# Optimization experiments

Measured on AMD Instinct MI355X. Metric: run time of the kernel, lower is better.

The kernel has to match this reference:

```python
import jax, jax.numpy as jnp
import numpy as np

N_PAPER = 200000
N_MESH = 30000
N = N_PAPER + N_MESH
D_PAPER = 512
D_MESH = 128
E_TRAIN = 2000000
E_POS = 500000
E_NEG = 500000


def setup_inputs() -> dict:
    key = jax.random.key(0)
    ks = jax.random.split(key, 32)

    def w(k, shape, fan_in):
        return jax.random.normal(k, shape, jnp.float32) / np.float32(np.sqrt(fan_in))

    inp = {}
    inp['x_paper'] = jax.random.normal(ks[0], (N_PAPER, D_PAPER), jnp.float32)
    inp['x_mesh'] = jax.random.normal(ks[1], (N_MESH, D_MESH), jnp.float32)
    # input transforms (stored as [in, out]; y = x @ W + b)
    inp['tp_w'] = w(ks[2], (D_PAPER, 16), D_PAPER)
    inp['tp_b'] = jnp.zeros((16,), jnp.float32)
    inp['tm_w'] = w(ks[3], (D_MESH, 16), D_MESH)
    inp['tm_b'] = jnp.zeros((16,), jnp.float32)
    # RGCN layers: basis decomposition W_r = sum_b comp[r,b] * basis[b]
    inp['comp1'] = w(ks[4], (2, 4), 4)
    inp['basis1'] = w(ks[5], (4, 16, 32), 16)
    inp['root1'] = w(ks[6], (16, 32), 16)
    inp['bias1'] = jnp.zeros((32,), jnp.float32)
    inp['comp2'] = w(ks[7], (2, 4), 4)
    inp['basis2'] = w(ks[8], (4, 32, 32), 32)
    inp['root2'] = w(ks[9], (32, 32), 32)
    inp['bias2'] = jnp.zeros((32,), jnp.float32)
    inp['comp3'] = w(ks[10], (2, 4), 4)
    inp['basis3'] = w(ks[11], (4, 32, 16), 32)
    inp['root3'] = w(ks[12], (32, 16), 32)
    inp['bias3'] = jnp.zeros((16,), jnp.float32)
    # decode linears (16 -> 16)
    inp['dpp_w'] = w(ks[13], (16, 16), 16)
    inp['dpp_b'] = jnp.zeros((16,), jnp.float32)
    inp['dpm_w'] = w(ks[14], (16, 16), 16)
    inp['dpm_b'] = jnp.zeros((16,), jnp.float32)
    # graph structure
    inp['train_edge_index'] = jax.random.randint(ks[15], (2, E_TRAIN), 0, N, jnp.int64)
    inp['train_edge_type'] = jax.random.randint(ks[16], (E_TRAIN,), 0, 2, jnp.int64)
    inp['pos_edge_index'] = jax.random.randint(ks[17], (2, E_POS), 0, N, jnp.int64)
    inp['pos_edge_type'] = jnp.sort(jax.random.randint(ks[18], (E_POS,), 0, 2, jnp.int64))
    inp['neg_edge_index'] = jax.random.randint(ks[19], (2, E_NEG), 0, N, jnp.int64)
    inp['neg_edge_type'] = jnp.sort(jax.random.randint(ks[20], (E_NEG,), 0, 2, jnp.int64))
    return inp


def rgcn(x, src, dst, etype, comp, basis, root, bias):
    # W: [R, in, out] from basis decomposition
    W = jnp.einsum('rb,bio->rio', comp, basis)
    # relation-typed message per edge (R == 2: compute both, select)
    xs = x[src]                                   # [E, in]  gather
    m = jnp.where((etype == 0)[:, None], xs @ W[0], xs @ W[1])  # [E, out]
    n = x.shape[0]
    agg = jax.ops.segment_sum(m, dst, num_segments=n)           # scatter-add
    deg = jax.ops.segment_sum(jnp.ones((src.shape[0],), x.dtype), dst, num_segments=n)
    agg = agg / jnp.maximum(deg, 1.0)[:, None]                   # mean aggregation
    return agg + x @ root + bias


def reference(x_paper, x_mesh, tp_w, tp_b, tm_w, tm_b,
              comp1, basis1, root1, bias1,
              comp2, basis2, root2, bias2,
              comp3, basis3, root3, bias3,
              dpp_w, dpp_b, dpm_w, dpm_b,
              train_edge_index, train_edge_type,
              pos_edge_index, pos_edge_type,
              neg_edge_index, neg_edge_type):
    # encode
    x = jnp.concatenate([x_paper @ tp_w + tp_b, x_mesh @ tm_w + tm_b], axis=0)
    src, dst = train_edge_index[0], train_edge_index[1]
    x = jax.nn.relu(rgcn(x, src, dst, train_edge_type, comp1, basis1, root1, bias1))
    x = jax.nn.relu(rgcn(x, src, dst, train_edge_type, comp2, basis2, root2, bias2))
    z = rgcn(x, src, dst, train_edge_type, comp3, basis3, root3, bias3)

    # decode: edge types are sorted, so per-edge type-select equals the
    # original mask-then-concat ordering [type0 ..., type1 ...]
    def edge_scores(ei, et):
        zs, zd = z[ei[0]], z[ei[1]]
        p = jnp.where((et == 0)[:, None], zs @ dpp_w + dpp_b, zs @ dpm_w + dpm_b)
        return (p * zd).sum(-1)

    return jnp.concatenate([edge_scores(pos_edge_index, pos_edge_type),
                            edge_scores(neg_edge_index, neg_edge_type)], axis=0)
```

## Files before the change

kernel.cpp:

```cpp
#include <hip/hip_runtime.h>

#define NPAPER 200000
#define NMESH  30000
#define NNODES 230000
#define ETRAIN 2000000
#define EPOS   500000
#define ENEG   500000

typedef _Float16 f16;
typedef __attribute__((ext_vector_type(8))) _Float16 f16x8;
typedef __attribute__((ext_vector_type(4))) _Float16 f16x4;

__device__ __forceinline__ void fma4(float4& a, float s, const float4 w) {
    a.x = fmaf(s, w.x, a.x);
    a.y = fmaf(s, w.y, a.y);
    a.z = fmaf(s, w.z, a.z);
    a.w = fmaf(s, w.w, a.w);
}

template <int D>
__global__ __launch_bounds__(256) void encode_kernel(
    const float* __restrict__ x, const float* __restrict__ w,
    const float* __restrict__ bias, float* __restrict__ out, int nrows) {
    constexpr int KP = 16;
    __shared__ float wlds[D * 16];
    __shared__ float xlds[256 * 20];
    __shared__ float blds[16];

    for (int i = threadIdx.x; i < D * 4; i += 256)
        reinterpret_cast<float4*>(wlds)[i] =
            reinterpret_cast<const float4*>(w)[i];
    if (threadIdx.x < 16) blds[threadIdx.x] = bias[threadIdx.x];

    const int g = threadIdx.x & 3;
    const int rg = threadIdx.x >> 2;
    const int row0 = blockIdx.x * 256;

    float4 acc[4];
#pragma unroll
    for (int j = 0; j < 4; j++) acc[j] = make_float4(0.f, 0.f, 0.f, 0.f);

    for (int p = 0; p < D / KP; p++) {
        __syncthreads();
        for (int i = threadIdx.x; i < 1024; i += 256) {
            const int rr = i >> 2, q = i & 3;
            const int grow = min(row0 + rr, nrows - 1);
            *reinterpret_cast<float4*>(xlds + rr * 20 + q * 4) =
                *reinterpret_cast<const float4*>(x + (size_t)grow * D +
                                                 p * KP + q * 4);
        }
        __syncthreads();
#pragma unroll
        for (int q = 0; q < KP / 4; q++) {
            const int k = p * KP + q * 4;
            const float4 w0 =
                *reinterpret_cast<const float4*>(wlds + (k + 0) * 16 + 4 * g);
            const float4 w1 =
                *reinterpret_cast<const float4*>(wlds + (k + 1) * 16 + 4 * g);
            const float4 w2 =
                *reinterpret_cast<const float4*>(wlds + (k + 2) * 16 + 4 * g);
            const float4 w3 =
                *reinterpret_cast<const float4*>(wlds + (k + 3) * 16 + 4 * g);
#pragma unroll
            for (int j = 0; j < 4; j++) {
                const float4 xv = *reinterpret_cast<const float4*>(
                    xlds + (rg + 64 * j) * 20 + q * 4);
                fma4(acc[j], xv.x, w0);
                fma4(acc[j], xv.y, w1);
                fma4(acc[j], xv.z, w2);
                fma4(acc[j], xv.w, w3);
            }
        }
    }

    const float4 b4 = *reinterpret_cast<const float4*>(blds + 4 * g);
#pragma unroll
    for (int j = 0; j < 4; j++) {
        const int grow = row0 + rg + 64 * j;
        if (grow < nrows) {
            float4 o;
            o.x = acc[j].x + b4.x;
            o.y = acc[j].y + b4.y;
            o.z = acc[j].z + b4.z;
            o.w = acc[j].w + b4.w;
            *reinterpret_cast<float4*>(out + (size_t)grow * 16 + 4 * g) = o;
        }
    }
}

__global__ __launch_bounds__(256) void hist_kernel(const int* __restrict__ dst,
                                                   int* __restrict__ cnt) {
    const int e = blockIdx.x * 256 + threadIdx.x;
    if (e >= ETRAIN) return;
    atomicAdd(cnt + dst[e], 1);
}

__global__ __launch_bounds__(256) void scan1_kernel(const int* __restrict__ in,
                                                    int* __restrict__ out,
                                                    int* __restrict__ bsum,
                                                    int n) {
    __shared__ int s[256];
    const int tid = threadIdx.x;
    const int i = blockIdx.x * 256 + tid;
    const int v = (i < n) ? in[i] : 0;
    s[tid] = v;
    __syncthreads();
#pragma unroll
    for (int off = 1; off < 256; off <<= 1) {
        const int t = (tid >= off) ? s[tid - off] : 0;
        __syncthreads();
        s[tid] += t;
        __syncthreads();
    }
    if (i < n) out[i] = s[tid] - v;
    if (tid == 255) bsum[blockIdx.x] = s[255];
}

__global__ __launch_bounds__(256) void scan2_kernel(int* __restrict__ bsum,
                                                    int nb) {
    __shared__ int s[256];
    const int tid = threadIdx.x;
    int carry = 0;
    for (int base = 0; base < nb; base += 256) {
        const int i = base + tid;
        const int v = (i < nb) ? bsum[i] : 0;
        s[tid] = v;
        __syncthreads();
#pragma unroll
        for (int off = 1; off < 256; off <<= 1) {
            const int t = (tid >= off) ? s[tid - off] : 0;
            __syncthreads();
            s[tid] += t;
            __syncthreads();
        }
        if (i < nb) bsum[i] = s[tid] - v + carry;
        const int tot = s[255];
        __syncthreads();
        carry += tot;
    }
}

__global__ __launch_bounds__(256) void scan3_kernel(int* __restrict__ out,
                                                    const int* __restrict__ bsum,
                                                    int n) {
    const int i = blockIdx.x * 256 + threadIdx.x;
    if (i < n) out[i] += bsum[blockIdx.x];
}

__global__ __launch_bounds__(256) void fill_kernel(
    const int* __restrict__ src, const int* __restrict__ dst,
    const int* __restrict__ et, const int* __restrict__ rowptr,
    int* __restrict__ fc, int* __restrict__ esorted) {
    const int e = blockIdx.x * 256 + threadIdx.x;
    if (e >= ETRAIN) return;
    const int d = dst[e];
    const int pos = rowptr[d] + atomicAdd(fc + d, 1);
    esorted[pos] = src[e] | (et[e] << 24);
}

template <int IN, bool XH>
__global__ __launch_bounds__(256) void agg_kernel(
    const void* __restrict__ xv, const int* __restrict__ rowptr,
    const int* __restrict__ cnt, const int* __restrict__ esorted,
    float* __restrict__ sx) {
    constexpr int NF = XH ? 8 : 4;
    const int gtid = blockIdx.x * 256 + threadIdx.x;
    const int n = gtid >> 4;
    if (n >= NNODES) return;
    const int lane = gtid & 15;
    const int f = lane & 3;
    const int e = lane >> 2;
    const int b = rowptr[n], c = cnt[n];

    float a0[NF], a1[NF];
#pragma unroll
    for (int j = 0; j < NF; j++) {
        a0[j] = 0.f;
        a1[j] = 0.f;
    }

    if constexpr (XH) {
        const f16* x = (const f16*)xv;
        for (int i = e; i < c; i += 4) {
            const int pk = esorted[b + i];
            const int s = pk & 0x00FFFFFF;
            const float w1 = (float)(pk >> 24);
            const float w0 = 1.0f - w1;
            const f16x8 raw = *((const f16x8*)(x + (size_t)s * IN) + f);
#pragma unroll
            for (int j = 0; j < 8; j++) {
                const float xf = (float)raw[j];
                a0[j] = fmaf(w0, xf, a0[j]);
                a1[j] = fmaf(w1, xf, a1[j]);
            }
        }
    } else {
        const float* x = (const float*)xv;
        for (int i = e; i < c; i += 4) {
            const int pk = esorted[b + i];
            const int s = pk & 0x00FFFFFF;
            const float w1 = (float)(pk >> 24);
            const float w0 = 1.0f - w1;
            const float4 xvv = *((const float4*)(x + (size_t)s * IN) + f);
            const float xf[4] = {xvv.x, xvv.y, xvv.z, xvv.w};
#pragma unroll
            for (int j = 0; j < 4; j++) {
                a0[j] = fmaf(w0, xf[j], a0[j]);
                a1[j] = fmaf(w1, xf[j], a1[j]);
            }
        }
    }
#pragma unroll
    for (int m = 4; m <= 8; m <<= 1) {
#pragma unroll
        for (int j = 0; j < NF; j++) {
            a0[j] += __shfl_xor(a0[j], m);
            a1[j] += __shfl_xor(a1[j], m);
        }
    }
    const float inv = 1.0f / fmaxf((float)c, 1.0f);
    float4* o = reinterpret_cast<float4*>(sx + (size_t)n * 2 * IN);
    if constexpr (XH) {
        float4 v;
        if (e == 0) v = make_float4(a0[0], a0[1], a0[2], a0[3]);
        else if (e == 1) v = make_float4(a0[4], a0[5], a0[6], a0[7]);
        else if (e == 2) v = make_float4(a1[0], a1[1], a1[2], a1[3]);
        else v = make_float4(a1[4], a1[5], a1[6], a1[7]);
        v.x *= inv; v.y *= inv; v.z *= inv; v.w *= inv;
        const int half = e >> 1, sub = e & 1;
        o[half * 8 + 2 * f + sub] = v;
    } else {
        if (e < 2) {
            float4 v;
            if (e == 0) v = make_float4(a0[0], a0[1], a0[2], a0[3]);
            else v = make_float4(a1[0], a1[1], a1[2], a1[3]);
            v.x *= inv; v.y *= inv; v.z *= inv; v.w *= inv;
            o[e * 4 + f] = v;
        }
    }
}

template <int IN, int OUT, bool RELU, bool INH, bool OUTH>
__global__ __launch_bounds__(256) void combine2_kernel(
    const void* __restrict__ xinp, const float* __restrict__ sx,
    const float* __restrict__ comp, const float* __restrict__ basis,
    const float* __restrict__ root, const float* __restrict__ bias,
    void* __restrict__ outp) {
    constexpr int QP = OUT / 4;
    __shared__ float wl[3 * IN * OUT];
    __shared__ float bl[OUT];
    for (int i = threadIdx.x; i < 2 * IN * OUT; i += 256) {
        const int r = i / (IN * OUT);
        const int rem = i - r * IN * OUT;
        float v = 0.f;
#pragma unroll
        for (int bb = 0; bb < 4; bb++)
            v = fmaf(comp[r * 4 + bb], basis[bb * IN * OUT + rem], v);
        wl[i] = v;
    }
    for (int i = threadIdx.x; i < IN * OUT; i += 256)
        wl[2 * IN * OUT + i] = root[i];
    if (threadIdx.x < OUT) bl[threadIdx.x] = bias[threadIdx.x];
    __syncthreads();

    const int gtid = blockIdx.x * 256 + threadIdx.x;
    const int n = gtid / QP;
    const int g = gtid % QP;
    if (n >= NNODES) return;

    float4 acc = *reinterpret_cast<const float4*>(bl + 4 * g);

    const float4* iv1 =
        reinterpret_cast<const float4*>(sx + (size_t)n * (2 * IN));
#pragma unroll
    for (int q = 0; q < 2 * IN / 4; q++) {
        const float4 xv = iv1[q];
        const float* wr = wl + (q * 4) * OUT + 4 * g;
        fma4(acc, xv.x, *reinterpret_cast<const float4*>(wr));
        fma4(acc, xv.y, *reinterpret_cast<const float4*>(wr + OUT));
        fma4(acc, xv.z, *reinterpret_cast<const float4*>(wr + 2 * OUT));
        fma4(acc, xv.w, *reinterpret_cast<const float4*>(wr + 3 * OUT));
    }
    if constexpr (INH) {
        const f16* xin = (const f16*)xinp;
        const f16x8* iv2 = (const f16x8*)(xin + (size_t)n * IN);
#pragma unroll
        for (int q = 0; q < IN / 8; q++) {
            const f16x8 raw = iv2[q];
            const float* wr = wl + (2 * IN + q * 8) * OUT + 4 * g;
#pragma unroll
            for (int j = 0; j < 8; j++)
                fma4(acc, (float)raw[j],
                     *reinterpret_cast<const float4*>(wr + j * OUT));
        }
    } else {
        const float4* iv2 =
            reinterpret_cast<const float4*>((const float*)xinp + (size_t)n * IN);
#pragma unroll
        for (int q = 0; q < IN / 4; q++) {
            const float4 xv = iv2[q];
            const float* wr = wl + (2 * IN + q * 4) * OUT + 4 * g;
            fma4(acc, xv.x, *reinterpret_cast<const float4*>(wr));
            fma4(acc, xv.y, *reinterpret_cast<const float4*>(wr + OUT));
            fma4(acc, xv.z, *reinterpret_cast<const float4*>(wr + 2 * OUT));
            fma4(acc, xv.w, *reinterpret_cast<const float4*>(wr + 3 * OUT));
        }
    }
    if (RELU) {
        acc.x = fmaxf(acc.x, 0.f);
        acc.y = fmaxf(acc.y, 0.f);
        acc.z = fmaxf(acc.z, 0.f);
        acc.w = fmaxf(acc.w, 0.f);
    }
    if constexpr (OUTH) {
        f16x4 hv;
        hv[0] = (f16)acc.x;
        hv[1] = (f16)acc.y;
        hv[2] = (f16)acc.z;
        hv[3] = (f16)acc.w;
        reinterpret_cast<f16x4*>((f16*)outp + (size_t)n * OUT)[g] = hv;
    } else {
        reinterpret_cast<float4*>((float*)outp + (size_t)n * OUT)[g] = acc;
    }
}

__global__ __launch_bounds__(256) void decode_kernel(
    const float* __restrict__ z, const int* __restrict__ ei,
    const int* __restrict__ et, const float* __restrict__ wp,
    const float* __restrict__ bp, const float* __restrict__ wm,
    const float* __restrict__ bm, float* __restrict__ out, int E) {
    __shared__ float wl[2 * 256];
    __shared__ float bl[2 * 16];
    {
        const int i = threadIdx.x;
        wl[i] = wp[i];
        wl[256 + i] = wm[i];
        if (i < 16) {
            bl[i] = bp[i];
            bl[16 + i] = bm[i];
        }
    }
    __syncthreads();

    const int gtid = blockIdx.x * 256 + threadIdx.x;
    const int e = gtid >> 2;
    const int f = gtid & 3;
    if (e >= E) return;
    const int s = ei[e], d = ei[e + E], t = et[e];

    const float4 zs = reinterpret_cast<const float4*>(z + (size_t)s * 16)[f];
    const float4 zd = reinterpret_cast<const float4*>(z + (size_t)d * 16)[f];

    const float* W = wl + t * 256;
    float4 p[4];
    if (f == 0) {
#pragma unroll
        for (int g = 0; g < 4; g++)
            p[g] = reinterpret_cast<const float4*>(bl + t * 16)[g];
    } else {
#pragma unroll
        for (int g = 0; g < 4; g++) p[g] = make_float4(0.f, 0.f, 0.f, 0.f);
    }
    const float xs[4] = {zs.x, zs.y, zs.z, zs.w};
#pragma unroll
    for (int c = 0; c < 4; c++) {
        const float4* wr =
            reinterpret_cast<const float4*>(W + (4 * f + c) * 16);
#pragma unroll
        for (int g = 0; g < 4; g++) fma4(p[g], xs[c], wr[g]);
    }
    float* pp = reinterpret_cast<float*>(p);
#pragma unroll
    for (int m = 1; m <= 2; m <<= 1) {
#pragma unroll
        for (int j = 0; j < 16; j++) pp[j] += __shfl_xor(pp[j], m);
    }
    float4 pf;
    if (f == 0) pf = p[0];
    else if (f == 1) pf = p[1];
    else if (f == 2) pf = p[2];
    else pf = p[3];
    float sc = pf.x * zd.x + pf.y * zd.y + pf.z * zd.z + pf.w * zd.w;
    sc += __shfl_xor(sc, 1);
    sc += __shfl_xor(sc, 2);
    if (f == 0) out[e] = sc;
}

extern "C" void kernel_launch(void* const* d_in, const int* in_sizes, int n_in,
                              void* d_out, int out_size, void* d_ws,
                              size_t ws_size, hipStream_t stream) {
    const float* x_paper = (const float*)d_in[0];
    const float* x_mesh = (const float*)d_in[1];
    const float* tp_w = (const float*)d_in[2];
    const float* tp_b = (const float*)d_in[3];
    const float* tm_w = (const float*)d_in[4];
    const float* tm_b = (const float*)d_in[5];
    const float* comp1 = (const float*)d_in[6];
    const float* basis1 = (const float*)d_in[7];
    const float* root1 = (const float*)d_in[8];
    const float* bias1 = (const float*)d_in[9];
    const float* comp2 = (const float*)d_in[10];
    const float* basis2 = (const float*)d_in[11];
    const float* root2 = (const float*)d_in[12];
    const float* bias2 = (const float*)d_in[13];
    const float* comp3 = (const float*)d_in[14];
    const float* basis3 = (const float*)d_in[15];
    const float* root3 = (const float*)d_in[16];
    const float* bias3 = (const float*)d_in[17];
    const float* dpp_w = (const float*)d_in[18];
    const float* dpp_b = (const float*)d_in[19];
    const float* dpm_w = (const float*)d_in[20];
    const float* dpm_b = (const float*)d_in[21];
    const int* tei = (const int*)d_in[22];
    const int* tet = (const int*)d_in[23];
    const int* pei = (const int*)d_in[24];
    const int* pet = (const int*)d_in[25];
    const int* nei = (const int*)d_in[26];
    const int* net = (const int*)d_in[27];
    float* out = (float*)d_out;

    float* ws = (float*)d_ws;
    float* R1 = ws;
    float* R2 = R1 + (size_t)NNODES * 32;
    float* R3 = R2 + (size_t)NNODES * 32;
    float* xfeat = R2;
    f16* h1h = (f16*)R1;
    f16* h2h = (f16*)R2;
    float* sx = R3;
    float* z = R1;

    int* rowptr = (int*)(R3 + (size_t)NNODES * 64);
    int* ecnt = rowptr + NNODES;
    int* fc = ecnt + NNODES;
    int* esorted = fc + NNODES;
    int* bsum = esorted + ETRAIN;

    const int* tsrc = tei;
    const int* tdst = tei + ETRAIN;

    const int eblocks = (ETRAIN + 255) / 256;
    const int nb = (NNODES + 255) / 256;
    const int aggb = (NNODES * 16 + 255) / 256;

    encode_kernel<512><<<(NPAPER + 255) / 256, 256, 0, stream>>>(
        x_paper, tp_w, tp_b, xfeat, NPAPER);
    encode_kernel<128><<<(NMESH + 255) / 256, 256, 0, stream>>>(
        x_mesh, tm_w, tm_b, xfeat + (size_t)NPAPER * 16, NMESH);

    hipMemsetAsync(ecnt, 0, (size_t)NNODES * 4, stream);
    hipMemsetAsync(fc, 0, (size_t)NNODES * 4, stream);
    hist_kernel<<<eblocks, 256, 0, stream>>>(tdst, ecnt);
    scan1_kernel<<<nb, 256, 0, stream>>>(ecnt, rowptr, bsum, NNODES);
    scan2_kernel<<<1, 256, 0, stream>>>(bsum, nb);
    scan3_kernel<<<nb, 256, 0, stream>>>(rowptr, bsum, NNODES);
    fill_kernel<<<eblocks, 256, 0, stream>>>(tsrc, tdst, tet, rowptr, fc,
                                             esorted);

    agg_kernel<16, false><<<aggb, 256, 0, stream>>>(xfeat, rowptr, ecnt,
                                                    esorted, sx);
    combine2_kernel<16, 32, true, false, true>
        <<<(NNODES * 8 + 255) / 256, 256, 0, stream>>>(xfeat, sx, comp1,
                                                       basis1, root1, bias1,
                                                       h1h);
    agg_kernel<32, true><<<aggb, 256, 0, stream>>>(h1h, rowptr, ecnt, esorted,
                                                   sx);
    combine2_kernel<32, 32, true, true, true>
        <<<(NNODES * 8 + 255) / 256, 256, 0, stream>>>(h1h, sx, comp2, basis2,
                                                       root2, bias2, h2h);
    agg_kernel<32, true><<<aggb, 256, 0, stream>>>(h2h, rowptr, ecnt, esorted,
                                                   sx);
    combine2_kernel<32, 16, false, true, false>
        <<<(NNODES * 4 + 255) / 256, 256, 0, stream>>>(h2h, sx, comp3, basis3,
                                                       root3, bias3, z);

    decode_kernel<<<(EPOS * 4 + 255) / 256, 256, 0, stream>>>(
        z, pei, pet, dpp_w, dpp_b, dpm_w, dpm_b, out, EPOS);
    decode_kernel<<<(ENEG * 4 + 255) / 256, 256, 0, stream>>>(
        z, nei, net, dpp_w, dpp_b, dpm_w, dpm_b, out + EPOS, ENEG);
}
```

Before: 1.158 ms.

## Transform node features before aggregation and gather pre-multiplied per-relation rows

Reorders each RGCN layer so every node is first multiplied by both relation weights and the root weight, written as fp16 per-relation rows. A following kernel gathers the row matching each edge's relation, averages, and adds the root term, bias and ReLU. Edge gathers thus read one relation-specific row instead of accumulating two weighted copies of the input, and the separate combine pass over aggregated sums goes away. It also folds the scan3 pass into consumers via bsum lookups, merges the two memsets and the two decode launches, and prefetches the next edge index in the gather loop. In exchange the layer-1 gather row grows (32 fp16 values instead of 16 fp32), and the per-relation transform output is stored in fp16, which changes rounding.

```diff
diff --git a/kernel.cpp b/kernel.cpp
--- a/kernel.cpp
+++ b/kernel.cpp
@@ -140,122 +140,34 @@
     }
 }
 
-__global__ __launch_bounds__(256) void scan3_kernel(int* __restrict__ out,
-                                                    const int* __restrict__ bsum,
-                                                    int n) {
-    const int i = blockIdx.x * 256 + threadIdx.x;
-    if (i < n) out[i] += bsum[blockIdx.x];
-}
-
 __global__ __launch_bounds__(256) void fill_kernel(
     const int* __restrict__ src, const int* __restrict__ dst,
     const int* __restrict__ et, const int* __restrict__ rowptr,
-    int* __restrict__ fc, int* __restrict__ esorted) {
+    const int* __restrict__ bsum, int* __restrict__ fc,
+    int* __restrict__ esorted) {
     const int e = blockIdx.x * 256 + threadIdx.x;
     if (e >= ETRAIN) return;
     const int d = dst[e];
-    const int pos = rowptr[d] + atomicAdd(fc + d, 1);
+    const int pos = rowptr[d] + bsum[d >> 8] + atomicAdd(fc + d, 1);
     esorted[pos] = src[e] | (et[e] << 24);
 }
 
-template <int IN, bool XH>
-__global__ __launch_bounds__(256) void agg_kernel(
-    const void* __restrict__ xv, const int* __restrict__ rowptr,
-    const int* __restrict__ cnt, const int* __restrict__ esorted,
-    float* __restrict__ sx) {
-    constexpr int NF = XH ? 8 : 4;
-    const int gtid = blockIdx.x * 256 + threadIdx.x;
-    const int n = gtid >> 4;
-    if (n >= NNODES) return;
-    const int lane = gtid & 15;
-    const int f = lane & 3;
-    const int e = lane >> 2;
-    const int b = rowptr[n], c = cnt[n];
-
-    float a0[NF], a1[NF];
-#pragma unroll
-    for (int j = 0; j < NF; j++) {
-        a0[j] = 0.f;
-        a1[j] = 0.f;
-    }
-
-    if constexpr (XH) {
-        const f16* x = (const f16*)xv;
-        for (int i = e; i < c; i += 4) {
-            const int pk = esorted[b + i];
-            const int s = pk & 0x00FFFFFF;
-            const float w1 = (float)(pk >> 24);
-            const float w0 = 1.0f - w1;
-            const f16x8 raw = *((const f16x8*)(x + (size_t)s * IN) + f);
-#pragma unroll
-            for (int j = 0; j < 8; j++) {
-                const float xf = (float)raw[j];
-                a0[j] = fmaf(w0, xf, a0[j]);
-                a1[j] = fmaf(w1, xf, a1[j]);
-            }
-        }
-    } else {
-        const float* x = (const float*)xv;
-        for (int i = e; i < c; i += 4) {
-            const int pk = esorted[b + i];
-            const int s = pk & 0x00FFFFFF;
-            const float w1 = (float)(pk >> 24);
-            const float w0 = 1.0f - w1;
-            const float4 xvv = *((const float4*)(x + (size_t)s * IN) + f);
-            const float xf[4] = {xvv.x, xvv.y, xvv.z, xvv.w};
-#pragma unroll
-            for (int j = 0; j < 4; j++) {
-                a0[j] = fmaf(w0, xf[j], a0[j]);
-                a1[j] = fmaf(w1, xf[j], a1[j]);
-            }
-        }
-    }
-#pragma unroll
-    for (int m = 4; m <= 8; m <<= 1) {
-#pragma unroll
-        for (int j = 0; j < NF; j++) {
-            a0[j] += __shfl_xor(a0[j], m);
-            a1[j] += __shfl_xor(a1[j], m);
-        }
-    }
-    const float inv = 1.0f / fmaxf((float)c, 1.0f);
-    float4* o = reinterpret_cast<float4*>(sx + (size_t)n * 2 * IN);
-    if constexpr (XH) {
-        float4 v;
-        if (e == 0) v = make_float4(a0[0], a0[1], a0[2], a0[3]);
-        else if (e == 1) v = make_float4(a0[4], a0[5], a0[6], a0[7]);
-        else if (e == 2) v = make_float4(a1[0], a1[1], a1[2], a1[3]);
-        else v = make_float4(a1[4], a1[5], a1[6], a1[7]);
-        v.x *= inv; v.y *= inv; v.z *= inv; v.w *= inv;
-        const int half = e >> 1, sub = e & 1;
-        o[half * 8 + 2 * f + sub] = v;
-    } else {
-        if (e < 2) {
-            float4 v;
-            if (e == 0) v = make_float4(a0[0], a0[1], a0[2], a0[3]);
-            else v = make_float4(a1[0], a1[1], a1[2], a1[3]);
-            v.x *= inv; v.y *= inv; v.z *= inv; v.w *= inv;
-            o[e * 4 + f] = v;
-        }
-    }
-}
-
-template <int IN, int OUT, bool RELU, bool INH, bool OUTH>
-__global__ __launch_bounds__(256) void combine2_kernel(
-    const void* __restrict__ xinp, const float* __restrict__ sx,
-    const float* __restrict__ comp, const float* __restrict__ basis,
-    const float* __restrict__ root, const float* __restrict__ bias,
-    void* __restrict__ outp) {
+template <int IN, int OUT, bool INH>
+__global__ __launch_bounds__(256) void transform_kernel(
+    const void* __restrict__ xinp, const float* __restrict__ comp,
+    const float* __restrict__ basis, const float* __restrict__ root,
+    const float* __restrict__ bias, f16* __restrict__ tcat,
+    float* __restrict__ rbuf) {
     constexpr int QP = OUT / 4;
     __shared__ float wl[3 * IN * OUT];
     __shared__ float bl[OUT];
     for (int i = threadIdx.x; i < 2 * IN * OUT; i += 256) {
-        const int r = i / (IN * OUT);
-        const int rem = i - r * IN * OUT;
+        const int rr = i / (IN * OUT);
+        const int rem = i - rr * IN * OUT;
         float v = 0.f;
 #pragma unroll
         for (int bb = 0; bb < 4; bb++)
-            v = fmaf(comp[r * 4 + bb], basis[bb * IN * OUT + rem], v);
+            v = fmaf(comp[rr * 4 + bb], basis[bb * IN * OUT + rem], v);
         wl[i] = v;
     }
     for (int i = threadIdx.x; i < IN * OUT; i += 256)
@@ -268,67 +180,160 @@
     const int g = gtid % QP;
     if (n >= NNODES) return;
 
-    float4 acc = *reinterpret_cast<const float4*>(bl + 4 * g);
-
-    const float4* iv1 =
-        reinterpret_cast<const float4*>(sx + (size_t)n * (2 * IN));
-#pragma unroll
-    for (int q = 0; q < 2 * IN / 4; q++) {
-        const float4 xv = iv1[q];
-        const float* wr = wl + (q * 4) * OUT + 4 * g;
-        fma4(acc, xv.x, *reinterpret_cast<const float4*>(wr));
-        fma4(acc, xv.y, *reinterpret_cast<const float4*>(wr + OUT));
-        fma4(acc, xv.z, *reinterpret_cast<const float4*>(wr + 2 * OUT));
-        fma4(acc, xv.w, *reinterpret_cast<const float4*>(wr + 3 * OUT));
-    }
+    float4 a0 = make_float4(0.f, 0.f, 0.f, 0.f);
+    float4 a1 = a0;
+    float4 ar = *reinterpret_cast<const float4*>(bl + 4 * g);
+
     if constexpr (INH) {
-        const f16* xin = (const f16*)xinp;
-        const f16x8* iv2 = (const f16x8*)(xin + (size_t)n * IN);
+        const f16* xin = (const f16*)xinp + (size_t)n * IN;
 #pragma unroll
         for (int q = 0; q < IN / 8; q++) {
-            const f16x8 raw = iv2[q];
-            const float* wr = wl + (2 * IN + q * 8) * OUT + 4 * g;
-#pragma unroll
-            for (int j = 0; j < 8; j++)
-                fma4(acc, (float)raw[j],
-                     *reinterpret_cast<const float4*>(wr + j * OUT));
+            const f16x8 raw = reinterpret_cast<const f16x8*>(xin)[q];
+#pragma unroll
+            for (int j = 0; j < 8; j++) {
+                const float xv = (float)raw[j];
+                const float* w0 = wl + (q * 8 + j) * OUT + 4 * g;
+                fma4(a0, xv, *reinterpret_cast<const float4*>(w0));
+                fma4(a1, xv, *reinterpret_cast<const float4*>(w0 + IN * OUT));
+                fma4(ar, xv,
+                     *reinterpret_cast<const float4*>(w0 + 2 * IN * OUT));
+            }
         }
     } else {
-        const float4* iv2 =
-            reinterpret_cast<const float4*>((const float*)xinp + (size_t)n * IN);
+        const float* xin = (const float*)xinp + (size_t)n * IN;
 #pragma unroll
         for (int q = 0; q < IN / 4; q++) {
-            const float4 xv = iv2[q];
-            const float* wr = wl + (2 * IN + q * 4) * OUT + 4 * g;
-            fma4(acc, xv.x, *reinterpret_cast<const float4*>(wr));
-            fma4(acc, xv.y, *reinterpret_cast<const float4*>(wr + OUT));
-            fma4(acc, xv.z, *reinterpret_cast<const float4*>(wr + 2 * OUT));
-            fma4(acc, xv.w, *reinterpret_cast<const float4*>(wr + 3 * OUT));
-        }
-    }
-    if (RELU) {
-        acc.x = fmaxf(acc.x, 0.f);
-        acc.y = fmaxf(acc.y, 0.f);
-        acc.z = fmaxf(acc.z, 0.f);
-        acc.w = fmaxf(acc.w, 0.f);
-    }
-    if constexpr (OUTH) {
-        f16x4 hv;
-        hv[0] = (f16)acc.x;
-        hv[1] = (f16)acc.y;
-        hv[2] = (f16)acc.z;
-        hv[3] = (f16)acc.w;
-        reinterpret_cast<f16x4*>((f16*)outp + (size_t)n * OUT)[g] = hv;
+            const float4 xv4 = reinterpret_cast<const float4*>(xin)[q];
+            const float xs[4] = {xv4.x, xv4.y, xv4.z, xv4.w};
+#pragma unroll
+            for (int j = 0; j < 4; j++) {
+                const float* w0 = wl + (q * 4 + j) * OUT + 4 * g;
+                fma4(a0, xs[j], *reinterpret_cast<const float4*>(w0));
+                fma4(a1, xs[j],
+                     *reinterpret_cast<const float4*>(w0 + IN * OUT));
+                fma4(ar, xs[j],
+                     *reinterpret_cast<const float4*>(w0 + 2 * IN * OUT));
+            }
+        }
+    }
+    f16x4 t0, t1;
+    t0[0] = (f16)a0.x; t0[1] = (f16)a0.y; t0[2] = (f16)a0.z; t0[3] = (f16)a0.w;
+    t1[0] = (f16)a1.x; t1[1] = (f16)a1.y; t1[2] = (f16)a1.z; t1[3] = (f16)a1.w;
+    f16* trow = tcat + (size_t)n * 2 * OUT;
+    reinterpret_cast<f16x4*>(trow)[g] = t0;
+    reinterpret_cast<f16x4*>(trow + OUT)[g] = t1;
+    reinterpret_cast<float4*>(rbuf + (size_t)n * OUT)[g] = ar;
+}
+
+template <int OUT, bool RELU, bool OUTH>
+__global__ __launch_bounds__(256) void aggroot_kernel(
+    const f16* __restrict__ tcat, const float* __restrict__ rbuf,
+    const int* __restrict__ rowptr, const int* __restrict__ bsum,
+    const int* __restrict__ cnt, const int* __restrict__ esorted,
+    void* __restrict__ outp) {
+    constexpr int NF = OUT / 4;
+    const int gtid = blockIdx.x * 256 + threadIdx.x;
+    const int n = gtid >> 5;
+    if (n >= NNODES) return;
+    const int lane = gtid & 31;
+    const int f = lane & 3;
+    const int e = lane >> 2;
+    const int b = rowptr[n] + bsum[n >> 8];
+    const int c = cnt[n];
+
+    float a[NF];
+#pragma unroll
+    for (int j = 0; j < NF; j++) a[j] = 0.f;
+
+    int i = e;
+    int pk = (i < c) ? esorted[b + i] : 0;
+    while (i < c) {
+        const int in2 = i + 8;
+        const int pkn = (in2 < c) ? esorted[b + in2] : 0;
+        const int s = pk & 0x00FFFFFF;
+        const int t = pk >> 24;
+        const f16* row = tcat + ((size_t)s * 2 + t) * OUT + f * NF;
+        if constexpr (NF == 8) {
+            const f16x8 raw = *reinterpret_cast<const f16x8*>(row);
+#pragma unroll
+            for (int j = 0; j < 8; j++) a[j] += (float)raw[j];
+        } else {
+            const f16x4 raw = *reinterpret_cast<const f16x4*>(row);
+#pragma unroll
+            for (int j = 0; j < 4; j++) a[j] += (float)raw[j];
+        }
+        pk = pkn;
+        i = in2;
+    }
+#pragma unroll
+    for (int m = 4; m <= 16; m <<= 1) {
+#pragma unroll
+        for (int j = 0; j < NF; j++) a[j] += __shfl_xor(a[j], m);
+    }
+    const float inv = 1.0f / fmaxf((float)c, 1.0f);
+    if constexpr (NF == 8) {
+        if (e < 2) {
+            const int off = f * 8 + e * 4;
+            const float4 rv =
+                *reinterpret_cast<const float4*>(rbuf + (size_t)n * OUT + off);
+            float4 v;
+            v.x = fmaf(a[e * 4 + 0], inv, rv.x);
+            v.y = fmaf(a[e * 4 + 1], inv, rv.y);
+            v.z = fmaf(a[e * 4 + 2], inv, rv.z);
+            v.w = fmaf(a[e * 4 + 3], inv, rv.w);
+            if (RELU) {
+                v.x = fmaxf(v.x, 0.f);
+                v.y = fmaxf(v.y, 0.f);
+                v.z = fmaxf(v.z, 0.f);
+                v.w = fmaxf(v.w, 0.f);
+            }
+            if constexpr (OUTH) {
+                f16x4 hv;
+                hv[0] = (f16)v.x; hv[1] = (f16)v.y;
+                hv[2] = (f16)v.z; hv[3] = (f16)v.w;
+                *reinterpret_cast<f16x4*>((f16*)outp + (size_t)n * OUT + off) =
+                    hv;
+            } else {
+                *reinterpret_cast<float4*>((float*)outp + (size_t)n * OUT +
+                                           off) = v;
+            }
+        }
     } else {
-        reinterpret_cast<float4*>((float*)outp + (size_t)n * OUT)[g] = acc;
+        if (e == 0) {
+            const int off = f * 4;
+            const float4 rv =
+                *reinterpret_cast<const float4*>(rbuf + (size_t)n * OUT + off);
+            float4 v;
+            v.x = fmaf(a[0], inv, rv.x);
+            v.y = fmaf(a[1], inv, rv.y);
+            v.z = fmaf(a[2], inv, rv.z);
+            v.w = fmaf(a[3], inv, rv.w);
+            if (RELU) {
+                v.x = fmaxf(v.x, 0.f);
+                v.y = fmaxf(v.y, 0.f);
+                v.z = fmaxf(v.z, 0.f);
+                v.w = fmaxf(v.w, 0.f);
+            }
+            if constexpr (OUTH) {
+                f16x4 hv;
+                hv[0] = (f16)v.x; hv[1] = (f16)v.y;
+                hv[2] = (f16)v.z; hv[3] = (f16)v.w;
+                *reinterpret_cast<f16x4*>((f16*)outp + (size_t)n * OUT + off) =
+                    hv;
+            } else {
+                *reinterpret_cast<float4*>((float*)outp + (size_t)n * OUT +
+                                           off) = v;
+            }
+        }
     }
 }
 
 __global__ __launch_bounds__(256) void decode_kernel(
-    const float* __restrict__ z, const int* __restrict__ ei,
-    const int* __restrict__ et, const float* __restrict__ wp,
+    const float* __restrict__ z, const int* __restrict__ pei,
+    const int* __restrict__ pet, const int* __restrict__ nei,
+    const int* __restrict__ net, const float* __restrict__ wp,
     const float* __restrict__ bp, const float* __restrict__ wm,
-    const float* __restrict__ bm, float* __restrict__ out, int E) {
+    const float* __restrict__ bm, float* __restrict__ out) {
     __shared__ float wl[2 * 256];
     __shared__ float bl[2 * 16];
     {
@@ -345,8 +350,18 @@
     const int gtid = blockIdx.x * 256 + threadIdx.x;
     const int e = gtid >> 2;
     const int f = gtid & 3;
-    if (e >= E) return;
-    const int s = ei[e], d = ei[e + E], t = et[e];
+    if (e >= EPOS + ENEG) return;
+    int s, d, t;
+    if (e < EPOS) {
+        s = pei[e];
+        d = pei[e + EPOS];
+        t = pet[e];
+    } else {
+        const int ee = e - EPOS;
+        s = nei[ee];
+        d = nei[ee + ENEG];
+        t = net[ee];
+    }
 
     const float4 zs = reinterpret_cast<const float4*>(z + (size_t)s * 16)[f];
     const float4 zd = reinterpret_cast<const float4*>(z + (size_t)d * 16)[f];
@@ -419,20 +434,18 @@
     const int* net = (const int*)d_in[27];
     float* out = (float*)d_out;
 
+    const size_t N = NNODES;
     float* ws = (float*)d_ws;
-    float* R1 = ws;
-    float* R2 = R1 + (size_t)NNODES * 32;
-    float* R3 = R2 + (size_t)NNODES * 32;
-    float* xfeat = R2;
-    f16* h1h = (f16*)R1;
-    f16* h2h = (f16*)R2;
-    float* sx = R3;
-    float* z = R1;
-
-    int* rowptr = (int*)(R3 + (size_t)NNODES * 64);
-    int* ecnt = rowptr + NNODES;
-    int* fc = ecnt + NNODES;
-    int* esorted = fc + NNODES;
+    float* xfeat = ws;
+    float* z = ws + 16 * N;
+    float* rbuf = ws + 32 * N;
+    f16* tcat = (f16*)(ws + 64 * N);
+    f16* h1 = (f16*)(ws + 96 * N);
+    f16* h2 = (f16*)(ws + 112 * N);
+    int* rowptr = (int*)(ws + 128 * N);
+    int* ecnt = rowptr + N;
+    int* fc = ecnt + N;
+    int* esorted = fc + N;
     int* bsum = esorted + ETRAIN;
 
     const int* tsrc = tei;
@@ -440,41 +453,41 @@
 
     const int eblocks = (ETRAIN + 255) / 256;
     const int nb = (NNODES + 255) / 256;
-    const int aggb = (NNODES * 16 + 255) / 256;
+    const int aggb = (NNODES * 32 + 255) / 256;
 
     encode_kernel<512><<<(NPAPER + 255) / 256, 256, 0, stream>>>(
         x_paper, tp_w, tp_b, xfeat, NPAPER);
     encode_kernel<128><<<(NMESH + 255) / 256, 256, 0, stream>>>(
         x_mesh, tm_w, tm_b, xfeat + (size_t)NPAPER * 16, NMESH);
 
-    hipMemsetAsync(ecnt, 0, (size_t)NNODES * 4, stream);
-    hipMemsetAsync(fc, 0, (size_t)NNODES * 4, stream);
+    hipMemsetAsync(ecnt, 0, (size_t)2 * NNODES * 4, stream);
     hist_kernel<<<eblocks, 256, 0, stream>>>(tdst, ecnt);
     scan1_kernel<<<nb, 256, 0, stream>>>(ecnt, rowptr, bsum, NNODES);
     scan2_kernel<<<1, 256, 0, stream>>>(bsum, nb);
-    scan3_kernel<<<nb, 256, 0, stream>>>(rowptr, bsum, NNODES);
-    fill_kernel<<<eblocks, 256, 0, stream>>>(tsrc, tdst, tet, rowptr, fc,
-                                             esorted);
-
-    agg_kernel<16, false><<<aggb, 256, 0, stream>>>(xfeat, rowptr, ecnt,
-                                                    esorted, sx);
-    combine2_kernel<16, 32, true, false, true>
-        <<<(NNODES * 8 + 255) / 256, 256, 0, stream>>>(xfeat, sx, comp1,
-                                                       basis1, root1, bias1,
-                                                       h1h);
-    agg_kernel<32, true><<<aggb, 256, 0, stream>>>(h1h, rowptr, ecnt, esorted,
-                                                   sx);
-    combine2_kernel<32, 32, true, true, true>
-        <<<(NNODES * 8 + 255) / 256, 256, 0, stream>>>(h1h, sx, comp2, basis2,
-                                                       root2, bias2, h2h);
-    agg_kernel<32, true><<<aggb, 256, 0, stream>>>(h2h, rowptr, ecnt, esorted,
-                                                   sx);
-    combine2_kernel<32, 16, false, true, false>
-        <<<(NNODES * 4 + 255) / 256, 256, 0, stream>>>(h2h, sx, comp3, basis3,
-                                                       root3, bias3, z);
-
-    decode_kernel<<<(EPOS * 4 + 255) / 256, 256, 0, stream>>>(
-        z, pei, pet, dpp_w, dpp_b, dpm_w, dpm_b, out, EPOS);
-    decode_kernel<<<(ENEG * 4 + 255) / 256, 256, 0, stream>>>(
-        z, nei, net, dpp_w, dpp_b, dpm_w, dpm_b, out + EPOS, ENEG);
-}
+    fill_kernel<<<eblocks, 256, 0, stream>>>(tsrc, tdst, tet, rowptr, bsum,
+                                             fc, esorted);
+
+    transform_kernel<16, 32, false>
+        <<<(NNODES * 8 + 255) / 256, 256, 0, stream>>>(xfeat, comp1, basis1,
+                                                       root1, bias1, tcat,
+                                                       rbuf);
+    aggroot_kernel<32, true, true><<<aggb, 256, 0, stream>>>(
+        tcat, rbuf, rowptr, bsum, ecnt, esorted, h1);
+
+    transform_kernel<32, 32, true>
+        <<<(NNODES * 8 + 255) / 256, 256, 0, stream>>>(h1, comp2, basis2,
+                                                       root2, bias2, tcat,
+                                                       rbuf);
+    aggroot_kernel<32, true, true><<<aggb, 256, 0, stream>>>(
+        tcat, rbuf, rowptr, bsum, ecnt, esorted, h2);
+
+    transform_kernel<32, 16, true>
+        <<<(NNODES * 4 + 255) / 256, 256, 0, stream>>>(h2, comp3, basis3,
+                                                       root3, bias3, tcat,
+                                                       rbuf);
+    aggroot_kernel<16, false, false><<<aggb, 256, 0, stream>>>(
+        tcat, rbuf, rowptr, bsum, ecnt, esorted, z);
+
+    decode_kernel<<<((EPOS + ENEG) * 4 + 255) / 256, 256, 0, stream>>>(
+        z, pei, pet, nei, net, dpp_w, dpp_b, dpm_w, dpm_b, out);
+}
```

After: 1.152 ms. About the same (-0.5%).
